# Optimization experiments

Hardware: AMD Instinct MI355X
Metric: run time of the kernel (lower is better)

The kernel has to match this reference:

```python
import jax, jax.numpy as jnp
import numpy as np

B, N, D, K = 512, 8192, 4096, 8  # B*K must equal D for the original .view to be valid
H = D // 2


def setup_inputs() -> dict:
    key = jax.random.key(0)
    ks = jax.random.split(key, 14)
    s = 1.0 / np.sqrt(D)
    inp = {
        "input_vector": jax.random.normal(ks[0], (B, D), jnp.float32),
        # learned parameters (all nodes active)
        "node_emb": jax.random.normal(ks[1], (N, D), jnp.float32) * 0.1,
        "adj": (jax.random.uniform(ks[2], (N, N), jnp.float32)
                * (jax.random.uniform(ks[3], (N, N), jnp.float32) < 0.01)),
        "Wq": jax.random.normal(ks[4], (D, D), jnp.float32) * s,
        "Wk": jax.random.normal(ks[5], (D, D), jnp.float32) * s,
        "W1": jax.random.normal(ks[6], (D, H), jnp.float32) * s,
        "b1": jnp.zeros((H,), jnp.float32),
        "W2": jax.random.normal(ks[7], (H, D), jnp.float32) * (1.0 / np.sqrt(H)),
        "b2": jnp.zeros((D,), jnp.float32),
        "Wc": jax.random.normal(ks[8], (D, 1), jnp.float32) * s,
        "Wo": jax.random.normal(ks[9], (D, D), jnp.float32) * s,
        "bo": jnp.zeros((D,), jnp.float32),
    }
    return inp


def reference(input_vector, node_emb, adj, Wq, Wk, W1, b1, W2, b2, Wc, Wo, bo):
    x = input_vector  # [B, D]
    # attention retrieval over active nodes (all N active)
    q = x @ Wq                                   # [B, D]
    keys = node_emb @ Wk                         # [N, D]
    scores = (q @ keys.T) / np.sqrt(D)           # [B, N]
    attn = jax.nn.softmax(scores, axis=-1)
    topk_w, topk_i = jax.lax.top_k(attn, K)     # [B, K]

    # vectorized bundle activation (faithful to original, needs B*K == D)
    sel = node_emb[topk_i]                       # [B, K, D]
    msg = adj[topk_i.reshape(-1)] @ node_emb     # [B*K, D]
    t = sel.reshape(-1, D) @ msg.T               # [B*K, B*K]
    bundle_inf = t.T.reshape(B, K, D)
    enh = sel + 0.1 * bundle_inf                 # [B, K, D]

    # activation MLP (exact GELU like torch default) + weighted aggregation
    h = jax.nn.gelu(enh @ W1 + b1, approximate=False) @ W2 + b2
    agg = (h * topk_w[..., None]).sum(axis=1)    # [B, D]

    final = (x + agg) @ Wo + bo                  # [B, D]
    conf = jax.nn.sigmoid(final @ Wc)            # [B, 1]
    return final, conf
```

## Files before the change

kernel.cpp:

```cpp
#include <hip/hip_runtime.h>
#include <hip/hip_bf16.h>
#include <math.h>

using bf16 = __hip_bfloat16;
using u8 = unsigned char;

typedef __attribute__((ext_vector_type(8))) short short8;
typedef __attribute__((ext_vector_type(4))) float f32x4;
typedef __attribute__((ext_vector_type(16))) float f32x16;
typedef __attribute__((ext_vector_type(4))) int int4v;
typedef __attribute__((ext_vector_type(8))) int int32x8;
typedef __attribute__((ext_vector_type(2))) unsigned int uint2v;

static constexpr int Bsz = 512, Nn = 8192, Dd = 4096, Hh = 2048;

enum { EPI_BF16 = 0, EPI_SCALE_F32, EPI_BIAS_BF16, EPI_BIAS_F32,
       EPI_FP8, EPI_ENH_FP8, EPI_GELU_FP8 };

__device__ __forceinline__ u8 f32_to_fp8(float x) {
  const unsigned int u = __float_as_uint(x);
  const unsigned int s = (u >> 24) & 0x80u;
  const float ax = fminf(__uint_as_float(u & 0x7fffffffu), 448.0f);
  const unsigned int au = __float_as_uint(ax);
  unsigned int b;
  if (au >= 0x3c800000u) {
    const unsigned int r = au + 0x7ffffu + ((au >> 20) & 1u);
    b = (((r >> 23) - 120u) << 3) | ((r >> 20) & 7u);
    if (b > 0x7eu) b = 0x7eu;
  } else {
    b = (unsigned int)(int)rintf(ax * 512.0f);
  }
  return (u8)(b | s);
}

__device__ __forceinline__ float fp8_to_f32(u8 b) {
  const int e = (b >> 3) & 15, m = b & 7;
  const float v = e ? __uint_as_float((unsigned)((e + 120) << 23) | ((unsigned)m << 20))
                    : (float)m * 0.001953125f;
  return (b & 0x80) ? -v : v;
}

__device__ __forceinline__ void gload_lds16(const void* g, void* l) {
  __builtin_amdgcn_global_load_lds(
      (const __attribute__((address_space(1))) void*)g,
      (__attribute__((address_space(3))) void*)l, 16, 0, 0);
}

__device__ __forceinline__ void stage_reg(const void* g, char* region,
                                          long grow0, long pitchB, long kbyte,
                                          int wave, int lane) {
  const int rl = lane >> 2, sl = lane & 3;
  const int s = sl ^ ((rl >> 1) & 3);
  const long r0 = (long)(wave << 5) + rl;
  const char* src0 = (const char*)g + (grow0 + r0) * pitchB + kbyte + (s << 4);
  gload_lds16(src0, region + (wave << 11));
  gload_lds16(src0 + 16 * pitchB, region + (wave << 11) + 1024);
}

#define VMCNT8 asm volatile("s_waitcnt vmcnt(8)" ::: "memory")

#define READ_AMX(DST, RG)                                                      \
  _Pragma("unroll") for (int mr = 0; mr < 2; ++mr) {                           \
    const int off0 = ((rowA + mr * 32) << 6) + lSw;                            \
    const int4v lo = *reinterpret_cast<const int4v*>((RG) + off0);             \
    const int4v hi = *reinterpret_cast<const int4v*>((RG) + (off0 ^ 16));      \
    DST[mr] = __builtin_shufflevector(lo, hi, 0, 1, 2, 3, 4, 5, 6, 7);         \
  }

#define READ_BMX(DST, RG)                                                      \
  _Pragma("unroll") for (int nr = 0; nr < 2; ++nr) {                           \
    const int off0 = ((rowB + nr * 32) << 6) + lSw;                            \
    const int4v lo = *reinterpret_cast<const int4v*>((RG) + off0);             \
    const int4v hi = *reinterpret_cast<const int4v*>((RG) + (off0 ^ 16));      \
    DST[nr] = __builtin_shufflevector(lo, hi, 0, 1, 2, 3, 4, 5, 6, 7);         \
  }

#define MFMA_MX(AV, BV)                                                        \
  __builtin_amdgcn_s_setprio(1);                                               \
  _Pragma("unroll") for (int mr = 0; mr < 2; ++mr)                             \
  _Pragma("unroll") for (int nr = 0; nr < 2; ++nr)                             \
    acc[mr][nr] = __builtin_amdgcn_mfma_scale_f32_32x32x64_f8f6f4(             \
        AV[mr], BV[nr], acc[mr][nr], 0, 0, 0, 0x7f7f7f7f, 0, 0x7f7f7f7f);      \
  __builtin_amdgcn_s_setprio(0);

template<int EPI>
__global__ __launch_bounds__(256, 2)
void gemm_mx(const u8* __restrict__ A, const u8* __restrict__ Bt,
             void* __restrict__ Cp, const u8* __restrict__ sel,
             const float* __restrict__ bias, float scale,
             int M, int N, int K)
{
  __shared__ char lds[65536];
  const int tid  = threadIdx.x;
  const int lane = tid & 63;
  const int wave = tid >> 6;
  const int wm = wave >> 1;
  const int wn = wave & 1;

  const int nblk = (M >> 7) * (N >> 7);
  const int q8 = nblk >> 3, r8 = nblk & 7;
  const int xcd = blockIdx.x & 7, pos = blockIdx.x >> 3;
  const int wg = (xcd < r8 ? xcd * (q8 + 1) : r8 * (q8 + 1) + (xcd - r8) * q8) + pos;
  const int ntx = N >> 7;
  const long bcol = (long)(wg % ntx) << 7;
  const long brow = (long)(wg / ntx) << 7;

  const int rowA = wm * 64 + (lane & 31);
  const int rowB = wn * 64 + (lane & 31);
  const int lSw = (((lane >> 5) ^ ((lane >> 2) & 1)) << 5) | (((lane >> 1) & 1) << 4);

  char* const Ar = (char*)lds;
  char* const Br = (char*)lds + 32768;

  f32x16 acc[2][2] = {};
  const int HT = K >> 6;

#pragma unroll
  for (int h = 0; h < 3; ++h) {
    stage_reg(Bt, Br + h * 8192, bcol, K, (long)h << 6, wave, lane);
    stage_reg(A,  Ar + h * 8192, brow, K, (long)h << 6, wave, lane);
  }
  VMCNT8;
  __builtin_amdgcn_s_barrier();

  for (int h = 0; h < HT; ++h) {
    const int hn = (h + 3 < HT) ? (h + 3) : (HT - 1);
    const int rg = (h + 3) & 3;
    stage_reg(Bt, Br + rg * 8192, bcol, K, (long)hn << 6, wave, lane);
    stage_reg(A,  Ar + rg * 8192, brow, K, (long)hn << 6, wave, lane);

    int32x8 aF[2], bF[2];
    READ_AMX(aF, Ar + (h & 3) * 8192);
    READ_BMX(bF, Br + (h & 3) * 8192);
    MFMA_MX(aF, bF);

    VMCNT8;
    __builtin_amdgcn_s_barrier();
  }

#pragma unroll
  for (int mr = 0; mr < 2; ++mr)
#pragma unroll
  for (int nr = 0; nr < 2; ++nr) {
    const long col = bcol + wn * 64 + nr * 32 + (lane & 31);
#pragma unroll
    for (int reg = 0; reg < 16; ++reg) {
      const long row = brow + wm * 64 + mr * 32 +
                       (reg & 3) + 8 * (reg >> 2) + 4 * (lane >> 5);
      const long idx = row * N + col;
      const float v = acc[mr][nr][reg];
      if constexpr (EPI == EPI_BF16) {
        reinterpret_cast<bf16*>(Cp)[idx] = __float2bfloat16(v);
      } else if constexpr (EPI == EPI_FP8) {
        reinterpret_cast<u8*>(Cp)[idx] = f32_to_fp8(v);
      } else if constexpr (EPI == EPI_ENH_FP8) {
        reinterpret_cast<u8*>(Cp)[idx] = f32_to_fp8(fp8_to_f32(sel[idx]) + 0.1f * v);
      } else if constexpr (EPI == EPI_GELU_FP8) {
        const float tt = v + bias[col];
        reinterpret_cast<u8*>(Cp)[idx] =
            f32_to_fp8(0.5f * tt * (1.0f + erff(tt * 0.7071067811865475f)));
      } else if constexpr (EPI == EPI_BIAS_BF16) {
        reinterpret_cast<bf16*>(Cp)[idx] = __float2bfloat16(v + bias[col]);
      } else {
        reinterpret_cast<float*>(Cp)[idx] = v + bias[col];
      }
    }
  }
}

template<int EPI>
__global__ __launch_bounds__(256)
void gemm_nt(const bf16* __restrict__ A, const bf16* __restrict__ Bt,
             void* __restrict__ Cp, const float* __restrict__ bias, float scale,
             int M, int N, int K)
{
  __shared__ bf16 As[128 * 64];
  __shared__ bf16 Bs[128 * 64];
  const int tid  = threadIdx.x;
  const int lane = tid & 63;
  const int wave = tid >> 6;
  const int wm = wave >> 1, wn = wave & 1;
  const long brow = (long)blockIdx.y * 128;
  const long bcol = (long)blockIdx.x * 128;

  f32x4 acc[4][4] = {};

  for (int k0 = 0; k0 < K; k0 += 64) {
    __syncthreads();
#pragma unroll
    for (int i = 0; i < 4; ++i) {
      const int s  = i * 256 + tid;
      const int r  = s >> 3;
      const int cs = s & 7;
      const int col = ((cs ^ (r & 7)) << 3);
      *reinterpret_cast<short8*>(&As[s << 3]) =
          *reinterpret_cast<const short8*>(&A[(brow + r) * K + k0 + col]);
      *reinterpret_cast<short8*>(&Bs[s << 3]) =
          *reinterpret_cast<const short8*>(&Bt[(bcol + r) * K + k0 + col]);
    }
    __syncthreads();
#pragma unroll
    for (int kk = 0; kk < 2; ++kk) {
      short8 af[4], bq[4];
      const int cc = (kk << 2) + (lane >> 4);
#pragma unroll
      for (int m = 0; m < 4; ++m) {
        const int r = wm * 64 + m * 16 + (lane & 15);
        af[m] = *reinterpret_cast<const short8*>(&As[((r << 3) + (cc ^ (r & 7))) << 3]);
      }
#pragma unroll
      for (int n = 0; n < 4; ++n) {
        const int r = wn * 64 + n * 16 + (lane & 15);
        bq[n] = *reinterpret_cast<const short8*>(&Bs[((r << 3) + (cc ^ (r & 7))) << 3]);
      }
#pragma unroll
      for (int m = 0; m < 4; ++m)
#pragma unroll
        for (int n = 0; n < 4; ++n)
          acc[m][n] = __builtin_amdgcn_mfma_f32_16x16x32_bf16(af[m], bq[n], acc[m][n], 0, 0, 0);
    }
  }

#pragma unroll
  for (int m = 0; m < 4; ++m) {
    const long row0 = brow + wm * 64 + m * 16 + ((lane >> 4) << 2);
#pragma unroll
    for (int n = 0; n < 4; ++n) {
      const long col = bcol + wn * 64 + n * 16 + (lane & 15);
#pragma unroll
      for (int j = 0; j < 4; ++j) {
        const long idx = (row0 + j) * N + col;
        const float v = acc[m][n][j];
        if constexpr (EPI == EPI_BF16) {
          reinterpret_cast<bf16*>(Cp)[idx] = __float2bfloat16(v);
        } else if constexpr (EPI == EPI_SCALE_F32) {
          reinterpret_cast<float*>(Cp)[idx] = v * scale;
        } else if constexpr (EPI == EPI_BIAS_BF16) {
          reinterpret_cast<bf16*>(Cp)[idx] = __float2bfloat16(v + bias[col]);
        } else if constexpr (EPI == EPI_BIAS_F32) {
          reinterpret_cast<float*>(Cp)[idx] = v + bias[col];
        }
      }
    }
  }
}

__global__ __launch_bounds__(256)
void k_convert_bf16(const float* __restrict__ in, bf16* __restrict__ out, long n4)
{
  const long i = (long)blockIdx.x * 256 + threadIdx.x;
  if (i >= n4) return;
  const f32x4 v = *reinterpret_cast<const f32x4*>(&in[i * 4]);
  bf16 o[4] __attribute__((aligned(8)));
#pragma unroll
  for (int j = 0; j < 4; ++j) o[j] = __float2bfloat16(v[j]);
  *reinterpret_cast<uint2v*>(&out[i * 4]) = *reinterpret_cast<uint2v*>(o);
}

__global__ __launch_bounds__(256)
void k_convert_fp8(const float* __restrict__ in, u8* __restrict__ out, long n4)
{
  const long i = (long)blockIdx.x * 256 + threadIdx.x;
  if (i >= n4) return;
  const f32x4 v = *reinterpret_cast<const f32x4*>(&in[i * 4]);
  u8 o[4] __attribute__((aligned(4)));
#pragma unroll
  for (int j = 0; j < 4; ++j) o[j] = f32_to_fp8(v[j]);
  *reinterpret_cast<unsigned int*>(&out[i * 4]) = *reinterpret_cast<unsigned int*>(o);
}

__global__ __launch_bounds__(256)
void k_transpose_bf16(const float* __restrict__ in, bf16* __restrict__ out, int R, int C)
{
  __shared__ float t[64][65];
  const int bc = blockIdx.x << 6;
  const int br = blockIdx.y << 6;
  for (int i = threadIdx.x; i < 4096; i += 256) {
    const int r = i >> 6, c = i & 63;
    t[r][c] = in[(long)(br + r) * C + (bc + c)];
  }
  __syncthreads();
  for (int i = threadIdx.x; i < 4096; i += 256) {
    const int r = i >> 6, c = i & 63;
    out[(long)(bc + r) * R + (br + c)] = __float2bfloat16(t[c][r]);
  }
}

__global__ __launch_bounds__(256)
void k_transpose_fp8(const float* __restrict__ in, u8* __restrict__ out, int R, int C)
{
  __shared__ float t[64][65];
  const int bc = blockIdx.x << 6;
  const int br = blockIdx.y << 6;
  for (int i = threadIdx.x; i < 4096; i += 256) {
    const int r = i >> 6, c = i & 63;
    t[r][c] = in[(long)(br + r) * C + (bc + c)];
  }
  __syncthreads();
  for (int i = threadIdx.x; i < 4096; i += 256) {
    const int r = i >> 6, c = i & 63;
    out[(long)(bc + r) * R + (br + c)] = f32_to_fp8(t[c][r]);
  }
}

__global__ __launch_bounds__(256)
void k_gather_fp8(const float* __restrict__ src, const int* __restrict__ map,
                  u8* __restrict__ dst, int cols)
{
  const long i = (long)blockIdx.x * 256 + threadIdx.x;
  const int cpr = cols >> 2;
  const int row = (int)(i / cpr);
  const int c4  = (int)(i % cpr) << 2;
  const f32x4 v = *reinterpret_cast<const f32x4*>(&src[(long)map[row] * cols + c4]);
  u8 o[4] __attribute__((aligned(4)));
#pragma unroll
  for (int j = 0; j < 4; ++j) o[j] = f32_to_fp8(v[j]);
  *reinterpret_cast<unsigned int*>(&dst[(long)row * cols + c4]) =
      *reinterpret_cast<unsigned int*>(o);
}

__global__ __launch_bounds__(256)
void k_gather_rows8(const u8* __restrict__ src, const int* __restrict__ map,
                    u8* __restrict__ dst, int cols)
{
  const long i = (long)blockIdx.x * 256 + threadIdx.x;
  const int cpr = cols >> 4;
  const int row = (int)(i / cpr);
  const int c16 = (int)(i % cpr) << 4;
  *reinterpret_cast<int4v*>(&dst[(long)row * cols + c16]) =
      *reinterpret_cast<const int4v*>(&src[(long)map[row] * cols + c16]);
}

__global__ __launch_bounds__(256)
void k_softmax_topk(const float* __restrict__ scores, int* __restrict__ tki,
                    float* __restrict__ tkw)
{
  const int b = blockIdx.x;
  const float* row = scores + (long)b * Nn;
  const int tid = threadIdx.x;
  __shared__ float red[8];
  __shared__ float cv[2048];
  __shared__ int   ci[2048];

  float mx = -INFINITY;
  for (int i = tid; i < Nn; i += 256) mx = fmaxf(mx, row[i]);
#pragma unroll
  for (int o = 32; o; o >>= 1) mx = fmaxf(mx, __shfl_down(mx, o));
  if ((tid & 63) == 0) red[tid >> 6] = mx;
  __syncthreads();
  mx = fmaxf(fmaxf(red[0], red[1]), fmaxf(red[2], red[3]));

  float tv[8]; int ti[8];
#pragma unroll
  for (int j = 0; j < 8; ++j) { tv[j] = -INFINITY; ti[j] = 0x7fffffff; }
  float sum = 0.f;
  for (int i = tid; i < Nn; i += 256) {
    const float v = row[i];
    sum += expf(v - mx);
    if (v > tv[7]) {
      tv[7] = v; ti[7] = i;
#pragma unroll
      for (int j = 7; j > 0; --j) {
        const bool sw = (tv[j] > tv[j-1]) || (tv[j] == tv[j-1] && ti[j] < ti[j-1]);
        if (sw) {
          const float fv = tv[j]; tv[j] = tv[j-1]; tv[j-1] = fv;
          const int   iv = ti[j]; ti[j] = ti[j-1]; ti[j-1] = iv;
        }
      }
    }
  }
  float s2 = sum;
#pragma unroll
  for (int o = 32; o; o >>= 1) s2 += __shfl_down(s2, o);
  if ((tid & 63) == 0) red[4 + (tid >> 6)] = s2;

#pragma unroll
  for (int j = 0; j < 8; ++j) { cv[tid * 8 + j] = tv[j]; ci[tid * 8 + j] = ti[j]; }
  __syncthreads();
  const float denom = red[4] + red[5] + red[6] + red[7];

  if (tid < 64) {
    for (int p = 0; p < 8; ++p) {
      float bv = -INFINITY; int bi = 0x7fffffff;
      for (int q = 0; q < 32; ++q) {
        const int slot = tid + (q << 6);
        const float v = cv[slot]; const int id = ci[slot];
        if (v > bv || (v == bv && id < bi)) { bv = v; bi = id; }
      }
#pragma unroll
      for (int o = 32; o; o >>= 1) {
        const float ov = __shfl_xor(bv, o);
        const int   oi = __shfl_xor(bi, o);
        if (ov > bv || (ov == bv && oi < bi)) { bv = ov; bi = oi; }
      }
      if (tid == 0) { tki[b * 8 + p] = bi; tkw[b * 8 + p] = expf(bv - mx) / denom; }
      for (int q = 0; q < 32; ++q) {
        const int slot = tid + (q << 6);
        if (ci[slot] == bi) cv[slot] = -INFINITY;
      }
    }
  }
}

__global__ __launch_bounds__(256)
void k_agg_xa(const float* __restrict__ x, const bf16* __restrict__ hout,
              const float* __restrict__ tkw, bf16* __restrict__ xa)
{
  const long i = (long)blockIdx.x * 256 + threadIdx.x;
  const int b = (int)(i >> 12);
  const int d = (int)(i & 4095);
  float a = x[i];
#pragma unroll
  for (int k = 0; k < 8; ++k)
    a += tkw[b * 8 + k] * __bfloat162float(hout[(((long)b * 8 + k) << 12) + d]);
  xa[i] = __float2bfloat16(a);
}

__global__ __launch_bounds__(256)
void k_conf(const float* __restrict__ fin, const float* __restrict__ Wc,
            float* __restrict__ conf)
{
  const int b = blockIdx.x;
  float s = 0.f;
  for (int d = threadIdx.x; d < Dd; d += 256)
    s += fin[(long)b * Dd + d] * Wc[d];
#pragma unroll
  for (int o = 32; o; o >>= 1) s += __shfl_down(s, o);
  __shared__ float r4[4];
  if ((threadIdx.x & 63) == 0) r4[threadIdx.x >> 6] = s;
  __syncthreads();
  if (threadIdx.x == 0) {
    const float t = r4[0] + r4[1] + r4[2] + r4[3];
    conf[b] = 1.f / (1.f + expf(-t));
  }
}

template<int EPI>
static inline void launch_gemm(const bf16* A, const bf16* Bt, void* C,
                               const float* bias, float scale,
                               int M, int N, int K, hipStream_t st)
{
  gemm_nt<EPI><<<dim3(N / 128, M / 128), 256, 0, st>>>(A, Bt, C, bias, scale, M, N, K);
}

template<int EPI>
static inline void launch_mx(const u8* A, const u8* Bt, void* C,
                             const u8* sel, const float* bias,
                             int M, int N, int K, hipStream_t st)
{
  gemm_mx<EPI><<<dim3((M >> 7) * (N >> 7)), 256, 0, st>>>(A, Bt, C, sel, bias, 1.f, M, N, K);
}

extern "C" void kernel_launch(void* const* d_in, const int* in_sizes, int n_in,
                              void* d_out, int out_size, void* d_ws, size_t ws_size,
                              hipStream_t stream)
{
  const float* x   = (const float*)d_in[0];
  const float* ne  = (const float*)d_in[1];
  const float* adj = (const float*)d_in[2];
  const float* Wq  = (const float*)d_in[3];
  const float* Wk  = (const float*)d_in[4];
  const float* W1  = (const float*)d_in[5];
  const float* b1  = (const float*)d_in[6];
  const float* W2  = (const float*)d_in[7];
  const float* b2  = (const float*)d_in[8];
  const float* Wc  = (const float*)d_in[9];
  const float* Wo  = (const float*)d_in[10];
  const float* bo  = (const float*)d_in[11];
  float* out = (float*)d_out;

  char* ws = (char*)d_ws;
  u8*    ne8   = (u8*)(ws);
  u8*    neT8  = (u8*)(ws + (32ll  << 20));
  u8*    adjG8 = (u8*)(ws + (64ll  << 20));
  bf16*  hout  = (bf16*)(ws + (64ll << 20));
  bf16*  keys  = (bf16*)(ws + (96ll  << 20));
  void*  slotW = (void*)(ws + (160ll << 20));
  u8*    sel8  = (u8*)(ws + (192ll << 20));
  u8*    msg8  = (u8*)(ws + (208ll << 20));
  u8*    hmid8 = msg8;
  float* scores= (float*)(ws + (224ll << 20));
  u8*    enh8  = (u8*)(ws + (224ll << 20));
  bf16*  xbf   = (bf16*)(ws + (240ll << 20));
  bf16*  qbf   = (bf16*)(ws + (244ll << 20));
  bf16*  xa    = (bf16*)(ws + (248ll << 20));
  int*   tki   = (int*)(ws + (252ll << 20));
  float* tkw   = (float*)(ws + (252ll << 20) + 16384);

  const long neN4 = (long)Nn * Dd / 4;
  const long xN4  = (long)Bsz * Dd / 4;

  k_convert_fp8<<<(int)(neN4 / 256), 256, 0, stream>>>(ne, ne8, neN4);
  k_transpose_fp8<<<dim3(64, 64), 256, 0, stream>>>(Wk, (u8*)slotW, Dd, Dd);
  launch_mx<EPI_BF16>(ne8, (u8*)slotW, keys, nullptr, nullptr, Nn, Dd, Dd, stream);
  k_convert_bf16<<<(int)(xN4 / 256), 256, 0, stream>>>(x, xbf, xN4);
  k_transpose_bf16<<<dim3(64, 64), 256, 0, stream>>>(Wq, (bf16*)slotW, Dd, Dd);
  launch_gemm<EPI_BF16>(xbf, (bf16*)slotW, qbf, nullptr, 1.f, Bsz, Dd, Dd, stream);
  launch_gemm<EPI_SCALE_F32>(qbf, keys, scores, nullptr, 1.f / 64.f, Bsz, Nn, Dd, stream);
  k_softmax_topk<<<Bsz, 256, 0, stream>>>(scores, tki, tkw);
  k_gather_rows8<<<(int)((long)4096 * Dd / 16 / 256), 256, 0, stream>>>(ne8, tki, sel8, Dd);
  k_gather_fp8<<<(int)((long)4096 * Nn / 4 / 256), 256, 0, stream>>>(adj, tki, adjG8, Nn);
  k_transpose_fp8<<<dim3(Dd / 64, Nn / 64), 256, 0, stream>>>(ne, neT8, Nn, Dd);
  launch_mx<EPI_FP8>(adjG8, neT8, msg8, nullptr, nullptr, 4096, Dd, Nn, stream);
  launch_mx<EPI_ENH_FP8>(msg8, sel8, enh8, sel8, nullptr, 4096, Dd, Dd, stream);
  k_transpose_fp8<<<dim3(Hh / 64, Dd / 64), 256, 0, stream>>>(W1, (u8*)slotW, Dd, Hh);
  launch_mx<EPI_GELU_FP8>(enh8, (u8*)slotW, hmid8, nullptr, b1, 4096, Hh, Dd, stream);
  k_transpose_fp8<<<dim3(Dd / 64, Hh / 64), 256, 0, stream>>>(W2, (u8*)slotW, Hh, Dd);
  launch_mx<EPI_BIAS_BF16>(hmid8, (u8*)slotW, hout, nullptr, b2, 4096, Dd, Hh, stream);
  k_agg_xa<<<(int)((long)Bsz * Dd / 256), 256, 0, stream>>>(x, hout, tkw, xa);
  k_transpose_bf16<<<dim3(64, 64), 256, 0, stream>>>(Wo, (bf16*)slotW, Dd, Dd);
  launch_gemm<EPI_BIAS_F32>(xa, (bf16*)slotW, out, bo, 1.f, Bsz, Dd, Dd, stream);
  k_conf<<<Bsz, 256, 0, stream>>>(out, Wc, out + (long)Bsz * Dd);
}
```

Baseline: 1.171 ms.

## Reassociate attention scores via Wq·Wkᵀ product and add 256-tile FP8 GEMM

The keys projection over all N nodes is replaced by precomputing P = Wq·Wkᵀ (a D×D FP8 GEMM), then computing x·P and scoring against node embeddings directly. This cuts the N×D×D keys GEMM down to a D×D×D one and moves the score and query GEMMs from bf16 to FP8. A new 512-thread, 256×256-tile MX GEMM kernel is added and used for the large message and enhancement GEMMs to improve data reuse. The cost is extra FP8 quantization of the Wq·Wkᵀ product and x·P, which may perturb top-k selection, and lower occupancy from the 128KB LDS tile.

```diff
diff --git a/kernel.cpp b/kernel.cpp
--- a/kernel.cpp
+++ b/kernel.cpp
@@ -59,29 +59,128 @@
 
 #define VMCNT8 asm volatile("s_waitcnt vmcnt(8)" ::: "memory")
 
-#define READ_AMX(DST, RG)                                                      \
+template<int EPI>
+__device__ __forceinline__ void epi_store(void* Cp, const u8* sel,
+                                          const float* bias, float scale,
+                                          long idx, long col, float v) {
+  if constexpr (EPI == EPI_BF16) {
+    reinterpret_cast<bf16*>(Cp)[idx] = __float2bfloat16(v);
+  } else if constexpr (EPI == EPI_SCALE_F32) {
+    reinterpret_cast<float*>(Cp)[idx] = v * scale;
+  } else if constexpr (EPI == EPI_FP8) {
+    reinterpret_cast<u8*>(Cp)[idx] = f32_to_fp8(v);
+  } else if constexpr (EPI == EPI_ENH_FP8) {
+    reinterpret_cast<u8*>(Cp)[idx] = f32_to_fp8(fp8_to_f32(sel[idx]) + 0.1f * v);
+  } else if constexpr (EPI == EPI_GELU_FP8) {
+    const float tt = v + bias[col];
+    reinterpret_cast<u8*>(Cp)[idx] =
+        f32_to_fp8(0.5f * tt * (1.0f + erff(tt * 0.7071067811865475f)));
+  } else if constexpr (EPI == EPI_BIAS_BF16) {
+    reinterpret_cast<bf16*>(Cp)[idx] = __float2bfloat16(v + bias[col]);
+  } else {
+    reinterpret_cast<float*>(Cp)[idx] = v + bias[col];
+  }
+}
+
+#define READ_AMX4(DST, RG)                                                     \
+  _Pragma("unroll") for (int mr = 0; mr < 4; ++mr) {                           \
+    const int off0 = ((rowA + mr * 32) << 6) + lSw;                            \
+    const int4v lo = *reinterpret_cast<const int4v*>((RG) + off0);             \
+    const int4v hi = *reinterpret_cast<const int4v*>((RG) + (off0 ^ 16));      \
+    DST[mr] = __builtin_shufflevector(lo, hi, 0, 1, 2, 3, 4, 5, 6, 7);         \
+  }
+
+#define READ_BMX2(DST, RG)                                                     \
+  _Pragma("unroll") for (int nr = 0; nr < 2; ++nr) {                           \
+    const int off0 = ((rowB + nr * 32) << 6) + lSw;                            \
+    const int4v lo = *reinterpret_cast<const int4v*>((RG) + off0);             \
+    const int4v hi = *reinterpret_cast<const int4v*>((RG) + (off0 ^ 16));      \
+    DST[nr] = __builtin_shufflevector(lo, hi, 0, 1, 2, 3, 4, 5, 6, 7);         \
+  }
+
+template<int EPI>
+__global__ __launch_bounds__(512, 1)
+void gemm_mx256(const u8* __restrict__ A, const u8* __restrict__ Bt,
+                void* __restrict__ Cp, const u8* __restrict__ sel,
+                const float* __restrict__ bias, float scale,
+                int M, int N, int K)
+{
+  __shared__ char lds[131072];
+  const int tid  = threadIdx.x;
+  const int lane = tid & 63;
+  const int wave = tid >> 6;
+  const int wm = wave >> 2;
+  const int wn = wave & 3;
+
+  const int nblk = (M >> 8) * (N >> 8);
+  const int q8 = nblk >> 3, r8 = nblk & 7;
+  const int xcd = blockIdx.x & 7, pos = blockIdx.x >> 3;
+  const int wg = (xcd < r8 ? xcd * (q8 + 1) : r8 * (q8 + 1) + (xcd - r8) * q8) + pos;
+  const int ntx = N >> 8;
+  const long bcol = (long)(wg % ntx) << 8;
+  const long brow = (long)(wg / ntx) << 8;
+
+  const int rowA = wm * 128 + (lane & 31);
+  const int rowB = wn * 64 + (lane & 31);
+  const int lSw = (((lane >> 5) ^ ((lane >> 2) & 1)) << 5) | (((lane >> 1) & 1) << 4);
+
+  char* const Ar = (char*)lds;
+  char* const Br = (char*)lds + 65536;
+
+  f32x16 acc[4][2] = {};
+  const int HT = K >> 6;
+
+#pragma unroll
+  for (int h = 0; h < 3; ++h) {
+    stage_reg(Bt, Br + h * 16384, bcol, K, (long)h << 6, wave, lane);
+    stage_reg(A,  Ar + h * 16384, brow, K, (long)h << 6, wave, lane);
+  }
+  VMCNT8;
+  __builtin_amdgcn_s_barrier();
+
+  for (int h = 0; h < HT; ++h) {
+    const int hn = (h + 3 < HT) ? (h + 3) : (HT - 1);
+    const int rg = (h + 3) & 3;
+    stage_reg(Bt, Br + rg * 16384, bcol, K, (long)hn << 6, wave, lane);
+    stage_reg(A,  Ar + rg * 16384, brow, K, (long)hn << 6, wave, lane);
+
+    int32x8 aF[4], bF[2];
+    READ_AMX4(aF, Ar + (h & 3) * 16384);
+    READ_BMX2(bF, Br + (h & 3) * 16384);
+    __builtin_amdgcn_s_setprio(1);
+#pragma unroll
+    for (int mr = 0; mr < 4; ++mr)
+#pragma unroll
+    for (int nr = 0; nr < 2; ++nr)
+      acc[mr][nr] = __builtin_amdgcn_mfma_scale_f32_32x32x64_f8f6f4(
+          aF[mr], bF[nr], acc[mr][nr], 0, 0, 0, 0x7f7f7f7f, 0, 0x7f7f7f7f);
+    __builtin_amdgcn_s_setprio(0);
+
+    VMCNT8;
+    __builtin_amdgcn_s_barrier();
+  }
+
+#pragma unroll
+  for (int mr = 0; mr < 4; ++mr)
+#pragma unroll
+  for (int nr = 0; nr < 2; ++nr) {
+    const long col = bcol + wn * 64 + nr * 32 + (lane & 31);
+#pragma unroll
+    for (int reg = 0; reg < 16; ++reg) {
+      const long row = brow + wm * 128 + mr * 32 +
+                       (reg & 3) + 8 * (reg >> 2) + 4 * (lane >> 5);
+      epi_store<EPI>(Cp, sel, bias, scale, row * N + col, col, acc[mr][nr][reg]);
+    }
+  }
+}
+
+#define READ_AMX2(DST, RG)                                                     \
   _Pragma("unroll") for (int mr = 0; mr < 2; ++mr) {                           \
     const int off0 = ((rowA + mr * 32) << 6) + lSw;                            \
     const int4v lo = *reinterpret_cast<const int4v*>((RG) + off0);             \
     const int4v hi = *reinterpret_cast<const int4v*>((RG) + (off0 ^ 16));      \
     DST[mr] = __builtin_shufflevector(lo, hi, 0, 1, 2, 3, 4, 5, 6, 7);         \
   }
-
-#define READ_BMX(DST, RG)                                                      \
-  _Pragma("unroll") for (int nr = 0; nr < 2; ++nr) {                           \
-    const int off0 = ((rowB + nr * 32) << 6) + lSw;                            \
-    const int4v lo = *reinterpret_cast<const int4v*>((RG) + off0);             \
-    const int4v hi = *reinterpret_cast<const int4v*>((RG) + (off0 ^ 16));      \
-    DST[nr] = __builtin_shufflevector(lo, hi, 0, 1, 2, 3, 4, 5, 6, 7);         \
-  }
-
-#define MFMA_MX(AV, BV)                                                        \
-  __builtin_amdgcn_s_setprio(1);                                               \
-  _Pragma("unroll") for (int mr = 0; mr < 2; ++mr)                             \
-  _Pragma("unroll") for (int nr = 0; nr < 2; ++nr)                             \
-    acc[mr][nr] = __builtin_amdgcn_mfma_scale_f32_32x32x64_f8f6f4(             \
-        AV[mr], BV[nr], acc[mr][nr], 0, 0, 0, 0x7f7f7f7f, 0, 0x7f7f7f7f);      \
-  __builtin_amdgcn_s_setprio(0);
 
 template<int EPI>
 __global__ __launch_bounds__(256, 2)
@@ -130,9 +229,16 @@
     stage_reg(A,  Ar + rg * 8192, brow, K, (long)hn << 6, wave, lane);
 
     int32x8 aF[2], bF[2];
-    READ_AMX(aF, Ar + (h & 3) * 8192);
-    READ_BMX(bF, Br + (h & 3) * 8192);
-    MFMA_MX(aF, bF);
+    READ_AMX2(aF, Ar + (h & 3) * 8192);
+    READ_BMX2(bF, Br + (h & 3) * 8192);
+    __builtin_amdgcn_s_setprio(1);
+#pragma unroll
+    for (int mr = 0; mr < 2; ++mr)
+#pragma unroll
+    for (int nr = 0; nr < 2; ++nr)
+      acc[mr][nr] = __builtin_amdgcn_mfma_scale_f32_32x32x64_f8f6f4(
+          aF[mr], bF[nr], acc[mr][nr], 0, 0, 0, 0x7f7f7f7f, 0, 0x7f7f7f7f);
+    __builtin_amdgcn_s_setprio(0);
 
     VMCNT8;
     __builtin_amdgcn_s_barrier();
@@ -147,32 +253,15 @@
     for (int reg = 0; reg < 16; ++reg) {
       const long row = brow + wm * 64 + mr * 32 +
                        (reg & 3) + 8 * (reg >> 2) + 4 * (lane >> 5);
-      const long idx = row * N + col;
-      const float v = acc[mr][nr][reg];
-      if constexpr (EPI == EPI_BF16) {
-        reinterpret_cast<bf16*>(Cp)[idx] = __float2bfloat16(v);
-      } else if constexpr (EPI == EPI_FP8) {
-        reinterpret_cast<u8*>(Cp)[idx] = f32_to_fp8(v);
-      } else if constexpr (EPI == EPI_ENH_FP8) {
-        reinterpret_cast<u8*>(Cp)[idx] = f32_to_fp8(fp8_to_f32(sel[idx]) + 0.1f * v);
-      } else if constexpr (EPI == EPI_GELU_FP8) {
-        const float tt = v + bias[col];
-        reinterpret_cast<u8*>(Cp)[idx] =
-            f32_to_fp8(0.5f * tt * (1.0f + erff(tt * 0.7071067811865475f)));
-      } else if constexpr (EPI == EPI_BIAS_BF16) {
-        reinterpret_cast<bf16*>(Cp)[idx] = __float2bfloat16(v + bias[col]);
-      } else {
-        reinterpret_cast<float*>(Cp)[idx] = v + bias[col];
-      }
-    }
-  }
-}
-
-template<int EPI>
-__global__ __launch_bounds__(256)
-void gemm_nt(const bf16* __restrict__ A, const bf16* __restrict__ Bt,
-             void* __restrict__ Cp, const float* __restrict__ bias, float scale,
-             int M, int N, int K)
+      epi_store<EPI>(Cp, sel, bias, scale, row * N + col, col, acc[mr][nr][reg]);
+    }
+  }
+}
+
+__global__ __launch_bounds__(256)
+void gemm_nt_final(const bf16* __restrict__ A, const bf16* __restrict__ Bt,
+                   float* __restrict__ Cp, const float* __restrict__ bias,
+                   int M, int N, int K)
 {
   __shared__ bf16 As[128 * 64];
   __shared__ bf16 Bs[128 * 64];
@@ -228,33 +317,10 @@
     for (int n = 0; n < 4; ++n) {
       const long col = bcol + wn * 64 + n * 16 + (lane & 15);
 #pragma unroll
-      for (int j = 0; j < 4; ++j) {
-        const long idx = (row0 + j) * N + col;
-        const float v = acc[m][n][j];
-        if constexpr (EPI == EPI_BF16) {
-          reinterpret_cast<bf16*>(Cp)[idx] = __float2bfloat16(v);
-        } else if constexpr (EPI == EPI_SCALE_F32) {
-          reinterpret_cast<float*>(Cp)[idx] = v * scale;
-        } else if constexpr (EPI == EPI_BIAS_BF16) {
-          reinterpret_cast<bf16*>(Cp)[idx] = __float2bfloat16(v + bias[col]);
-        } else if constexpr (EPI == EPI_BIAS_F32) {
-          reinterpret_cast<float*>(Cp)[idx] = v + bias[col];
-        }
-      }
-    }
-  }
-}
-
-__global__ __launch_bounds__(256)
-void k_convert_bf16(const float* __restrict__ in, bf16* __restrict__ out, long n4)
-{
-  const long i = (long)blockIdx.x * 256 + threadIdx.x;
-  if (i >= n4) return;
-  const f32x4 v = *reinterpret_cast<const f32x4*>(&in[i * 4]);
-  bf16 o[4] __attribute__((aligned(8)));
-#pragma unroll
-  for (int j = 0; j < 4; ++j) o[j] = __float2bfloat16(v[j]);
-  *reinterpret_cast<uint2v*>(&out[i * 4]) = *reinterpret_cast<uint2v*>(o);
+      for (int j = 0; j < 4; ++j)
+        Cp[(row0 + j) * N + col] = acc[m][n][j] + bias[col];
+    }
+  }
 }
 
 __global__ __launch_bounds__(256)
@@ -436,19 +502,19 @@
 }
 
 template<int EPI>
-static inline void launch_gemm(const bf16* A, const bf16* Bt, void* C,
-                               const float* bias, float scale,
-                               int M, int N, int K, hipStream_t st)
-{
-  gemm_nt<EPI><<<dim3(N / 128, M / 128), 256, 0, st>>>(A, Bt, C, bias, scale, M, N, K);
+static inline void launch_mx256(const u8* A, const u8* Bt, void* C,
+                                const u8* sel, const float* bias,
+                                int M, int N, int K, hipStream_t st)
+{
+  gemm_mx256<EPI><<<dim3((M >> 8) * (N >> 8)), 512, 0, st>>>(A, Bt, C, sel, bias, 1.f, M, N, K);
 }
 
 template<int EPI>
 static inline void launch_mx(const u8* A, const u8* Bt, void* C,
-                             const u8* sel, const float* bias,
+                             const u8* sel, const float* bias, float scale,
                              int M, int N, int K, hipStream_t st)
 {
-  gemm_mx<EPI><<<dim3((M >> 7) * (N >> 7)), 256, 0, st>>>(A, Bt, C, sel, bias, 1.f, M, N, K);
+  gemm_mx<EPI><<<dim3((M >> 7) * (N >> 7)), 256, 0, st>>>(A, Bt, C, sel, bias, scale, M, N, K);
 }
 
 extern "C" void kernel_launch(void* const* d_in, const int* in_sizes, int n_in,
@@ -474,41 +540,43 @@
   u8*    neT8  = (u8*)(ws + (32ll  << 20));
   u8*    adjG8 = (u8*)(ws + (64ll  << 20));
   bf16*  hout  = (bf16*)(ws + (64ll << 20));
-  bf16*  keys  = (bf16*)(ws + (96ll  << 20));
-  void*  slotW = (void*)(ws + (160ll << 20));
-  u8*    sel8  = (u8*)(ws + (192ll << 20));
-  u8*    msg8  = (u8*)(ws + (208ll << 20));
+  void*  slotW = (void*)(ws + (96ll  << 20));
+  u8*    Wq8   = (u8*)(ws + (128ll << 20));
+  u8*    Wk8   = (u8*)(ws + (144ll << 20));
+  u8*    PT8   = (u8*)(ws + (160ll << 20));
+  u8*    xP8   = (u8*)(ws + (176ll << 20));
+  float* scores= (float*)(ws + (180ll << 20));
+  u8*    sel8  = (u8*)(ws + (196ll << 20));
+  u8*    msg8  = (u8*)(ws + (212ll << 20));
   u8*    hmid8 = msg8;
-  float* scores= (float*)(ws + (224ll << 20));
-  u8*    enh8  = (u8*)(ws + (224ll << 20));
-  bf16*  xbf   = (bf16*)(ws + (240ll << 20));
-  bf16*  qbf   = (bf16*)(ws + (244ll << 20));
+  u8*    enh8  = (u8*)(ws + (228ll << 20));
+  u8*    x8    = (u8*)(ws + (244ll << 20));
   bf16*  xa    = (bf16*)(ws + (248ll << 20));
   int*   tki   = (int*)(ws + (252ll << 20));
   float* tkw   = (float*)(ws + (252ll << 20) + 16384);
 
-  const long neN4 = (long)Nn * Dd / 4;
-  const long xN4  = (long)Bsz * Dd / 4;
-
-  k_convert_fp8<<<(int)(neN4 / 256), 256, 0, stream>>>(ne, ne8, neN4);
-  k_transpose_fp8<<<dim3(64, 64), 256, 0, stream>>>(Wk, (u8*)slotW, Dd, Dd);
-  launch_mx<EPI_BF16>(ne8, (u8*)slotW, keys, nullptr, nullptr, Nn, Dd, Dd, stream);
-  k_convert_bf16<<<(int)(xN4 / 256), 256, 0, stream>>>(x, xbf, xN4);
-  k_transpose_bf16<<<dim3(64, 64), 256, 0, stream>>>(Wq, (bf16*)slotW, Dd, Dd);
-  launch_gemm<EPI_BF16>(xbf, (bf16*)slotW, qbf, nullptr, 1.f, Bsz, Dd, Dd, stream);
-  launch_gemm<EPI_SCALE_F32>(qbf, keys, scores, nullptr, 1.f / 64.f, Bsz, Nn, Dd, stream);
+  k_convert_fp8<<<(int)((long)Nn * Dd / 4 / 256), 256, 0, stream>>>(ne, ne8, (long)Nn * Dd / 4);
+  k_convert_fp8<<<(int)((long)Dd * Dd / 4 / 256), 256, 0, stream>>>(Wk, Wk8, (long)Dd * Dd / 4);
+  k_convert_fp8<<<(int)((long)Dd * Dd / 4 / 256), 256, 0, stream>>>(Wq, Wq8, (long)Dd * Dd / 4);
+  k_convert_fp8<<<(int)((long)Bsz * Dd / 4 / 256), 256, 0, stream>>>(x, x8, (long)Bsz * Dd / 4);
+
+  launch_mx256<EPI_FP8>(Wk8, Wq8, PT8, nullptr, nullptr, Dd, Dd, Dd, stream);
+  launch_mx<EPI_FP8>(x8, PT8, xP8, nullptr, nullptr, 1.f, Bsz, Dd, Dd, stream);
+  launch_mx<EPI_SCALE_F32>(xP8, ne8, scores, nullptr, nullptr, 1.f / 64.f,
+                           Bsz, Nn, Dd, stream);
   k_softmax_topk<<<Bsz, 256, 0, stream>>>(scores, tki, tkw);
   k_gather_rows8<<<(int)((long)4096 * Dd / 16 / 256), 256, 0, stream>>>(ne8, tki, sel8, Dd);
   k_gather_fp8<<<(int)((long)4096 * Nn / 4 / 256), 256, 0, stream>>>(adj, tki, adjG8, Nn);
   k_transpose_fp8<<<dim3(Dd / 64, Nn / 64), 256, 0, stream>>>(ne, neT8, Nn, Dd);
-  launch_mx<EPI_FP8>(adjG8, neT8, msg8, nullptr, nullptr, 4096, Dd, Nn, stream);
-  launch_mx<EPI_ENH_FP8>(msg8, sel8, enh8, sel8, nullptr, 4096, Dd, Dd, stream);
+  launch_mx256<EPI_FP8>(adjG8, neT8, msg8, nullptr, nullptr, 4096, Dd, Nn, stream);
+  launch_mx256<EPI_ENH_FP8>(msg8, sel8, enh8, sel8, nullptr, 4096, Dd, Dd, stream);
   k_transpose_fp8<<<dim3(Hh / 64, Dd / 64), 256, 0, stream>>>(W1, (u8*)slotW, Dd, Hh);
-  launch_mx<EPI_GELU_FP8>(enh8, (u8*)slotW, hmid8, nullptr, b1, 4096, Hh, Dd, stream);
+  launch_mx<EPI_GELU_FP8>(enh8, (u8*)slotW, hmid8, nullptr, b1, 1.f, 4096, Hh, Dd, stream);
   k_transpose_fp8<<<dim3(Dd / 64, Hh / 64), 256, 0, stream>>>(W2, (u8*)slotW, Hh, Dd);
-  launch_mx<EPI_BIAS_BF16>(hmid8, (u8*)slotW, hout, nullptr, b2, 4096, Dd, Hh, stream);
+  launch_mx<EPI_BIAS_BF16>(hmid8, (u8*)slotW, hout, nullptr, b2, 1.f, 4096, Dd, Hh, stream);
   k_agg_xa<<<(int)((long)Bsz * Dd / 256), 256, 0, stream>>>(x, hout, tkw, xa);
   k_transpose_bf16<<<dim3(64, 64), 256, 0, stream>>>(Wo, (bf16*)slotW, Dd, Dd);
-  launch_gemm<EPI_BIAS_F32>(xa, (bf16*)slotW, out, bo, 1.f, Bsz, Dd, Dd, stream);
+  gemm_nt_final<<<dim3(Dd / 128, Bsz / 128), 256, 0, stream>>>(
+      xa, (bf16*)slotW, out, bo, Bsz, Dd, Dd);
   k_conf<<<Bsz, 256, 0, stream>>>(out, Wc, out + (long)Bsz * Dd);
 }
```

Measured after the change: 942.2 us, median of 4. 1.24x faster.
